# Kernel optimization log

Hardware: AMD Instinct MI355X
Metric: run time of the kernel (lower is better)

The kernel has to match this reference:

```python
import jax, jax.numpy as jnp
import numpy as np

HARDNESS = 5.0

def setup_inputs() -> dict:
    key = jax.random.key(0)
    k1, k2 = jax.random.split(key)
    x = jax.random.normal(k1, (64, 8, 32, 32, 16), dtype=jnp.float32)
    ref = jax.random.normal(k2, (64, 16), dtype=jnp.float32)
    return {"input": x, "ref": ref}

def reference(input, ref):
    # Squared L2 distance from every element vector (last dim) to every codeword,
    x2 = jnp.sum(input * input, axis=-1)                      # (D1,D2,D3,D4)
    r2 = jnp.sum(ref * ref, axis=-1)                          # (M,)
    cross = jnp.einsum('abcde,me->mabcd', input, ref)         # (M,D1,D2,D3,D4)
    sq_l2 = x2[None] - 2.0 * cross + r2[:, None, None, None, None]
    # Softmax over codebook axis with -hardness temperature (dim=0 in torch).
    y = jax.nn.softmax(-HARDNESS * sq_l2, axis=0)             # (M,D1,D2,D3,D4)
    # Weighted combination of codewords.
    z = jnp.einsum('mabcd,me->abcde', y, ref)                 # (D1..D5)
    return z
```

## Files before the change

### kernel.cpp

```cpp
#include <hip/hip_runtime.h>
#include <math.h>

#define CB_M 64
#define CB_D 16
#define HARD 5.0f
#define LOG2E 1.44269504088896340736f

typedef __attribute__((ext_vector_type(8))) short bf16x8;
typedef __attribute__((ext_vector_type(4))) float f32x4;
typedef __attribute__((ext_vector_type(4))) int   i32x4;

#if __has_builtin(__builtin_amdgcn_exp2f)
#define EXP2F(x) __builtin_amdgcn_exp2f(x)
#else
#define EXP2F(x) exp2f(x)
#endif

#if __has_builtin(__builtin_amdgcn_rcpf)
#define RCPF(x) __builtin_amdgcn_rcpf(x)
#else
#define RCPF(x) (1.0f / (x))
#endif

__device__ __forceinline__ ushort f2bf_rne(float f) {
    unsigned u = __float_as_uint(f);
    u += 0x7fffu + ((u >> 16) & 1u);
    return (ushort)(u >> 16);
}
__device__ __forceinline__ float bf2f(ushort h) {
    return __uint_as_float(((unsigned)h) << 16);
}
__device__ __forceinline__ int pk(float a, float b) {
    return (int)__builtin_amdgcn_perm(__float_as_uint(a), __float_as_uint(b), 0x07060302u);
}
__device__ __forceinline__ float rnd(float a) {
    return __uint_as_float(__float_as_uint(a) + 0x8000u);
}
__device__ __forceinline__ float hi_trunc(float a) {
    return __uint_as_float(__float_as_uint(a) & 0xffff0000u);
}

__global__ __launch_bounds__(256, 4) void stq_main(const float* __restrict__ x,
                                                   const float* __restrict__ ref,
                                                   float* __restrict__ out,
                                                   int ntiles) {
    __shared__ __align__(16) float  cb_bias[CB_M];
    __shared__ __align__(16) ushort cb_rs_hi[CB_M][CB_D];
    __shared__ __align__(16) ushort cb_rs_lo[CB_M][CB_D];
    __shared__ __align__(16) ushort cb_rzT_hi[CB_D][CB_M];

    const int tid = threadIdx.x;

    if (tid < CB_M) {
        const f32x4* rp = (const f32x4*)(ref + tid * CB_D);
        f32x4 q0 = rp[0], q1 = rp[1], q2 = rp[2], q3 = rp[3];
        float r[CB_D] = {q0.x,q0.y,q0.z,q0.w, q1.x,q1.y,q1.z,q1.w,
                         q2.x,q2.y,q2.z,q2.w, q3.x,q3.y,q3.z,q3.w};
        float r2 = 0.0f;
#pragma unroll
        for (int j = 0; j < CB_D; ++j) r2 += r[j] * r[j];
        cb_bias[tid] = -(HARD * LOG2E) * r2;
        const float s = 2.0f * HARD * LOG2E;
#pragma unroll
        for (int j = 0; j < CB_D; ++j) {
            float v = s * r[j];
            ushort h = f2bf_rne(v);
            cb_rs_hi[tid][j] = h;
            cb_rs_lo[tid][j] = f2bf_rne(v - bf2f(h));
            cb_rzT_hi[j][tid] = f2bf_rne(r[j]);
        }
    }
    __syncthreads();

    const int lane = tid & 63;
    const int wid  = tid >> 6;
    const int i = lane & 15;
    const int c = lane >> 4;
    const bool hiquad = (c < 2);

    bf16x8 A1[4];
    f32x4  cinit[4];
#pragma unroll
    for (int t = 0; t < 4; ++t) {
        const int cwa = 32 * (t >> 1) + 8 * (i >> 2) + 4 * (t & 1) + (i & 3);
        const ushort* src = hiquad ? &cb_rs_hi[cwa][0] : &cb_rs_lo[cwa][0];
        A1[t] = *(const bf16x8*)(src + (c & 1) * 8);
#pragma unroll
        for (int r = 0; r < 4; ++r)
            cinit[t][r] = cb_bias[32 * (t >> 1) + 8 * c + 4 * (t & 1) + r];
    }
    bf16x8 BzH0 = *(const bf16x8*)&cb_rzT_hi[i][c * 8];
    bf16x8 BzH1 = *(const bf16x8*)&cb_rzT_hi[i][32 + c * 8];

    const int nwaves = gridDim.x * 4;
    int tile = blockIdx.x * 4 + wid;

    f32x4 nxa, nxb;
    {
        const float* xp = x + ((size_t)tile * 16 + i) * CB_D + (c & 1) * 8;
        nxa = *(const f32x4*)xp;
        nxb = *(const f32x4*)(xp + 4);
    }

#pragma unroll 1
    for (; tile < ntiles; tile += nwaves) {
        f32x4 xa = nxa, xb = nxb;
        const int nt = tile + nwaves;
        if (nt < ntiles) {
            const float* xp = x + ((size_t)nt * 16 + i) * CB_D + (c & 1) * 8;
            nxa = *(const f32x4*)xp;
            nxb = *(const f32x4*)(xp + 4);
        }

        i32x4 B1i, B2i;
        B1i.x = pk(xa.y, xa.x); B1i.y = pk(xa.w, xa.z);
        B1i.z = pk(xb.y, xb.x); B1i.w = pk(xb.w, xb.z);
        float l0 = xa.x - hi_trunc(xa.x), l1 = xa.y - hi_trunc(xa.y);
        float l2 = xa.z - hi_trunc(xa.z), l3 = xa.w - hi_trunc(xa.w);
        float l4 = xb.x - hi_trunc(xb.x), l5 = xb.y - hi_trunc(xb.y);
        float l6 = xb.z - hi_trunc(xb.z), l7 = xb.w - hi_trunc(xb.w);
        B2i.x = hiquad ? pk(rnd(l1), rnd(l0)) : 0;
        B2i.y = hiquad ? pk(rnd(l3), rnd(l2)) : 0;
        B2i.z = hiquad ? pk(rnd(l5), rnd(l4)) : 0;
        B2i.w = hiquad ? pk(rnd(l7), rnd(l6)) : 0;
        bf16x8 B1 = __builtin_bit_cast(bf16x8, B1i);
        bf16x8 B2 = __builtin_bit_cast(bf16x8, B2i);

        f32x4 acc[4];
#pragma unroll
        for (int t = 0; t < 4; ++t) {
            acc[t] = __builtin_amdgcn_mfma_f32_16x16x32_bf16(A1[t], B1, cinit[t], 0, 0, 0);
            acc[t] = __builtin_amdgcn_mfma_f32_16x16x32_bf16(A1[t], B2, acc[t], 0, 0, 0);
        }

        float lmax = acc[0][0];
#pragma unroll
        for (int t = 0; t < 4; ++t)
#pragma unroll
            for (int r = 0; r < 4; ++r) lmax = fmaxf(lmax, acc[t][r]);
        lmax = fmaxf(lmax, __shfl_xor(lmax, 16, 64));
        lmax = fmaxf(lmax, __shfl_xor(lmax, 32, 64));

        float lsum = 0.0f;
#pragma unroll
        for (int t = 0; t < 4; ++t)
#pragma unroll
            for (int r = 0; r < 4; ++r) {
                acc[t][r] = EXP2F(acc[t][r] - lmax);
                lsum += acc[t][r];
            }
        lsum += __shfl_xor(lsum, 16, 64);
        lsum += __shfl_xor(lsum, 32, 64);
        const float inv = RCPF(lsum);

        i32x4 P1i, P2i;
        P1i.x = pk(rnd(acc[0][1] * inv), rnd(acc[0][0] * inv));
        P1i.y = pk(rnd(acc[0][3] * inv), rnd(acc[0][2] * inv));
        P1i.z = pk(rnd(acc[1][1] * inv), rnd(acc[1][0] * inv));
        P1i.w = pk(rnd(acc[1][3] * inv), rnd(acc[1][2] * inv));
        P2i.x = pk(rnd(acc[2][1] * inv), rnd(acc[2][0] * inv));
        P2i.y = pk(rnd(acc[2][3] * inv), rnd(acc[2][2] * inv));
        P2i.z = pk(rnd(acc[3][1] * inv), rnd(acc[3][0] * inv));
        P2i.w = pk(rnd(acc[3][3] * inv), rnd(acc[3][2] * inv));
        bf16x8 P1 = __builtin_bit_cast(bf16x8, P1i);
        bf16x8 P2 = __builtin_bit_cast(bf16x8, P2i);

        f32x4 z = {0.0f, 0.0f, 0.0f, 0.0f};
        z = __builtin_amdgcn_mfma_f32_16x16x32_bf16(P1, BzH0, z, 0, 0, 0);
        z = __builtin_amdgcn_mfma_f32_16x16x32_bf16(P2, BzH1, z, 0, 0, 0);

        const int rowbase = tile * 16;
#pragma unroll
        for (int r = 0; r < 4; ++r)
            out[(size_t)(rowbase + 4 * c + r) * CB_D + i] = z[r];
    }
}

extern "C" void kernel_launch(void* const* d_in, const int* in_sizes, int n_in,
                              void* d_out, int out_size, void* d_ws, size_t ws_size,
                              hipStream_t stream) {
    const float* x   = (const float*)d_in[0];
    const float* ref = (const float*)d_in[1];
    float* out = (float*)d_out;

    const int nvec = in_sizes[0] / CB_D;
    const int ntiles = nvec / 16;

    stq_main<<<2048, 256, 0, stream>>>(x, ref, out, ntiles);
}
```

Measured before the change: 87.94 us.

## Process two tiles per wave iteration and defer softmax normalization to output

Each wave now handles a pair of 16-row tiles per loop iteration, interleaving their MFMAs and cross-lane reductions to expose more independent work. The softmax normalization moves from the probabilities to the final output: unnormalized exponentials are packed to bf16 by truncation, and the z results are scaled by a reciprocal fetched via shuffle. Rounding on the residual and probability packing is dropped, and the launch bound is lowered to 3 waves per SIMD to allow more registers. This trades some bf16 precision and occupancy for higher ILP and fewer VALU ops per tile, and an odd tile count would leave the last tile unprocessed.

```diff
diff --git a/kernel.cpp b/kernel.cpp
--- a/kernel.cpp
+++ b/kernel.cpp
@@ -33,14 +33,11 @@
 __device__ __forceinline__ int pk(float a, float b) {
     return (int)__builtin_amdgcn_perm(__float_as_uint(a), __float_as_uint(b), 0x07060302u);
 }
-__device__ __forceinline__ float rnd(float a) {
-    return __uint_as_float(__float_as_uint(a) + 0x8000u);
-}
 __device__ __forceinline__ float hi_trunc(float a) {
     return __uint_as_float(__float_as_uint(a) & 0xffff0000u);
 }
 
-__global__ __launch_bounds__(256, 4) void stq_main(const float* __restrict__ x,
+__global__ __launch_bounds__(256, 3) void stq_main(const float* __restrict__ x,
                                                    const float* __restrict__ ref,
                                                    float* __restrict__ out,
                                                    int ntiles) {
@@ -77,6 +74,7 @@
     const int i = lane & 15;
     const int c = lane >> 4;
     const bool hiquad = (c < 2);
+    const int  bmask = hiquad ? -1 : 0;
 
     bf16x8 A1[4];
     f32x4  cinit[4];
@@ -93,86 +91,128 @@
     bf16x8 BzH1 = *(const bf16x8*)&cb_rzT_hi[i][32 + c * 8];
 
     const int nwaves = gridDim.x * 4;
-    int tile = blockIdx.x * 4 + wid;
-
-    f32x4 nxa, nxb;
+    const int npairs = ntiles >> 1;
+    int p = blockIdx.x * 4 + wid;
+
+    f32x4 nx0a, nx0b, nx1a, nx1b;
     {
-        const float* xp = x + ((size_t)tile * 16 + i) * CB_D + (c & 1) * 8;
-        nxa = *(const f32x4*)xp;
-        nxb = *(const f32x4*)(xp + 4);
+        const float* xp = x + ((size_t)p * 32 + i) * CB_D + (c & 1) * 8;
+        nx0a = *(const f32x4*)xp;
+        nx0b = *(const f32x4*)(xp + 4);
+        nx1a = *(const f32x4*)(xp + 16 * CB_D);
+        nx1b = *(const f32x4*)(xp + 16 * CB_D + 4);
     }
 
 #pragma unroll 1
-    for (; tile < ntiles; tile += nwaves) {
-        f32x4 xa = nxa, xb = nxb;
-        const int nt = tile + nwaves;
-        if (nt < ntiles) {
-            const float* xp = x + ((size_t)nt * 16 + i) * CB_D + (c & 1) * 8;
-            nxa = *(const f32x4*)xp;
-            nxb = *(const f32x4*)(xp + 4);
-        }
-
-        i32x4 B1i, B2i;
-        B1i.x = pk(xa.y, xa.x); B1i.y = pk(xa.w, xa.z);
-        B1i.z = pk(xb.y, xb.x); B1i.w = pk(xb.w, xb.z);
-        float l0 = xa.x - hi_trunc(xa.x), l1 = xa.y - hi_trunc(xa.y);
-        float l2 = xa.z - hi_trunc(xa.z), l3 = xa.w - hi_trunc(xa.w);
-        float l4 = xb.x - hi_trunc(xb.x), l5 = xb.y - hi_trunc(xb.y);
-        float l6 = xb.z - hi_trunc(xb.z), l7 = xb.w - hi_trunc(xb.w);
-        B2i.x = hiquad ? pk(rnd(l1), rnd(l0)) : 0;
-        B2i.y = hiquad ? pk(rnd(l3), rnd(l2)) : 0;
-        B2i.z = hiquad ? pk(rnd(l5), rnd(l4)) : 0;
-        B2i.w = hiquad ? pk(rnd(l7), rnd(l6)) : 0;
-        bf16x8 B1 = __builtin_bit_cast(bf16x8, B1i);
-        bf16x8 B2 = __builtin_bit_cast(bf16x8, B2i);
-
-        f32x4 acc[4];
-#pragma unroll
-        for (int t = 0; t < 4; ++t) {
-            acc[t] = __builtin_amdgcn_mfma_f32_16x16x32_bf16(A1[t], B1, cinit[t], 0, 0, 0);
-            acc[t] = __builtin_amdgcn_mfma_f32_16x16x32_bf16(A1[t], B2, acc[t], 0, 0, 0);
-        }
-
-        float lmax = acc[0][0];
-#pragma unroll
-        for (int t = 0; t < 4; ++t)
-#pragma unroll
-            for (int r = 0; r < 4; ++r) lmax = fmaxf(lmax, acc[t][r]);
-        lmax = fmaxf(lmax, __shfl_xor(lmax, 16, 64));
-        lmax = fmaxf(lmax, __shfl_xor(lmax, 32, 64));
-
-        float lsum = 0.0f;
-#pragma unroll
-        for (int t = 0; t < 4; ++t)
-#pragma unroll
-            for (int r = 0; r < 4; ++r) {
-                acc[t][r] = EXP2F(acc[t][r] - lmax);
-                lsum += acc[t][r];
+    for (; p < npairs; p += nwaves) {
+        f32x4 xa0 = nx0a, xb0 = nx0b, xa1 = nx1a, xb1 = nx1b;
+        const int np_ = p + nwaves;
+        if (np_ < npairs) {
+            const float* xp = x + ((size_t)np_ * 32 + i) * CB_D + (c & 1) * 8;
+            nx0a = *(const f32x4*)xp;
+            nx0b = *(const f32x4*)(xp + 4);
+            nx1a = *(const f32x4*)(xp + 16 * CB_D);
+            nx1b = *(const f32x4*)(xp + 16 * CB_D + 4);
+        }
+
+        bf16x8 B1[2], B2[2];
+        {
+            i32x4 b1, b2;
+            b1.x = pk(xa0.y, xa0.x); b1.y = pk(xa0.w, xa0.z);
+            b1.z = pk(xb0.y, xb0.x); b1.w = pk(xb0.w, xb0.z);
+            b2.x = pk(xa0.y - hi_trunc(xa0.y), xa0.x - hi_trunc(xa0.x)) & bmask;
+            b2.y = pk(xa0.w - hi_trunc(xa0.w), xa0.z - hi_trunc(xa0.z)) & bmask;
+            b2.z = pk(xb0.y - hi_trunc(xb0.y), xb0.x - hi_trunc(xb0.x)) & bmask;
+            b2.w = pk(xb0.w - hi_trunc(xb0.w), xb0.z - hi_trunc(xb0.z)) & bmask;
+            B1[0] = __builtin_bit_cast(bf16x8, b1);
+            B2[0] = __builtin_bit_cast(bf16x8, b2);
+            b1.x = pk(xa1.y, xa1.x); b1.y = pk(xa1.w, xa1.z);
+            b1.z = pk(xb1.y, xb1.x); b1.w = pk(xb1.w, xb1.z);
+            b2.x = pk(xa1.y - hi_trunc(xa1.y), xa1.x - hi_trunc(xa1.x)) & bmask;
+            b2.y = pk(xa1.w - hi_trunc(xa1.w), xa1.z - hi_trunc(xa1.z)) & bmask;
+            b2.z = pk(xb1.y - hi_trunc(xb1.y), xb1.x - hi_trunc(xb1.x)) & bmask;
+            b2.w = pk(xb1.w - hi_trunc(xb1.w), xb1.z - hi_trunc(xb1.z)) & bmask;
+            B1[1] = __builtin_bit_cast(bf16x8, b1);
+            B2[1] = __builtin_bit_cast(bf16x8, b2);
+        }
+
+        f32x4 acc[2][4];
+#pragma unroll
+        for (int u = 0; u < 2; ++u)
+#pragma unroll
+            for (int t = 0; t < 4; ++t) {
+                acc[u][t] = __builtin_amdgcn_mfma_f32_16x16x32_bf16(A1[t], B1[u], cinit[t], 0, 0, 0);
+                acc[u][t] = __builtin_amdgcn_mfma_f32_16x16x32_bf16(A1[t], B2[u], acc[u][t], 0, 0, 0);
             }
-        lsum += __shfl_xor(lsum, 16, 64);
-        lsum += __shfl_xor(lsum, 32, 64);
-        const float inv = RCPF(lsum);
-
-        i32x4 P1i, P2i;
-        P1i.x = pk(rnd(acc[0][1] * inv), rnd(acc[0][0] * inv));
-        P1i.y = pk(rnd(acc[0][3] * inv), rnd(acc[0][2] * inv));
-        P1i.z = pk(rnd(acc[1][1] * inv), rnd(acc[1][0] * inv));
-        P1i.w = pk(rnd(acc[1][3] * inv), rnd(acc[1][2] * inv));
-        P2i.x = pk(rnd(acc[2][1] * inv), rnd(acc[2][0] * inv));
-        P2i.y = pk(rnd(acc[2][3] * inv), rnd(acc[2][2] * inv));
-        P2i.z = pk(rnd(acc[3][1] * inv), rnd(acc[3][0] * inv));
-        P2i.w = pk(rnd(acc[3][3] * inv), rnd(acc[3][2] * inv));
-        bf16x8 P1 = __builtin_bit_cast(bf16x8, P1i);
-        bf16x8 P2 = __builtin_bit_cast(bf16x8, P2i);
-
-        f32x4 z = {0.0f, 0.0f, 0.0f, 0.0f};
-        z = __builtin_amdgcn_mfma_f32_16x16x32_bf16(P1, BzH0, z, 0, 0, 0);
-        z = __builtin_amdgcn_mfma_f32_16x16x32_bf16(P2, BzH1, z, 0, 0, 0);
-
-        const int rowbase = tile * 16;
-#pragma unroll
-        for (int r = 0; r < 4; ++r)
-            out[(size_t)(rowbase + 4 * c + r) * CB_D + i] = z[r];
+
+        float lmax[2];
+#pragma unroll
+        for (int u = 0; u < 2; ++u) {
+            float m01 = fmaxf(fmaxf(acc[u][0][0], acc[u][0][1]), fmaxf(acc[u][0][2], acc[u][0][3]));
+            float m23 = fmaxf(fmaxf(acc[u][1][0], acc[u][1][1]), fmaxf(acc[u][1][2], acc[u][1][3]));
+            float m45 = fmaxf(fmaxf(acc[u][2][0], acc[u][2][1]), fmaxf(acc[u][2][2], acc[u][2][3]));
+            float m67 = fmaxf(fmaxf(acc[u][3][0], acc[u][3][1]), fmaxf(acc[u][3][2], acc[u][3][3]));
+            lmax[u] = fmaxf(fmaxf(m01, m23), fmaxf(m45, m67));
+        }
+        float s0a = __shfl_xor(lmax[0], 16, 64);
+        float s1a = __shfl_xor(lmax[1], 16, 64);
+        lmax[0] = fmaxf(lmax[0], s0a);
+        lmax[1] = fmaxf(lmax[1], s1a);
+        s0a = __shfl_xor(lmax[0], 32, 64);
+        s1a = __shfl_xor(lmax[1], 32, 64);
+        lmax[0] = fmaxf(lmax[0], s0a);
+        lmax[1] = fmaxf(lmax[1], s1a);
+
+        float lsum[2];
+#pragma unroll
+        for (int u = 0; u < 2; ++u) {
+            float s = 0.0f;
+#pragma unroll
+            for (int t = 0; t < 4; ++t)
+#pragma unroll
+                for (int r = 0; r < 4; ++r) {
+                    acc[u][t][r] = EXP2F(acc[u][t][r] - lmax[u]);
+                    s += acc[u][t][r];
+                }
+            lsum[u] = s;
+        }
+        s0a = __shfl_xor(lsum[0], 16, 64);
+        s1a = __shfl_xor(lsum[1], 16, 64);
+        lsum[0] += s0a;
+        lsum[1] += s1a;
+        s0a = __shfl_xor(lsum[0], 32, 64);
+        s1a = __shfl_xor(lsum[1], 32, 64);
+        float inv0 = RCPF(lsum[0] + s0a);
+        float inv1 = RCPF(lsum[1] + s1a);
+
+        f32x4 z[2];
+#pragma unroll
+        for (int u = 0; u < 2; ++u) {
+            i32x4 p1, p2;
+            p1.x = pk(acc[u][0][1], acc[u][0][0]);
+            p1.y = pk(acc[u][0][3], acc[u][0][2]);
+            p1.z = pk(acc[u][1][1], acc[u][1][0]);
+            p1.w = pk(acc[u][1][3], acc[u][1][2]);
+            p2.x = pk(acc[u][2][1], acc[u][2][0]);
+            p2.y = pk(acc[u][2][3], acc[u][2][2]);
+            p2.z = pk(acc[u][3][1], acc[u][3][0]);
+            p2.w = pk(acc[u][3][3], acc[u][3][2]);
+            bf16x8 P1 = __builtin_bit_cast(bf16x8, p1);
+            bf16x8 P2 = __builtin_bit_cast(bf16x8, p2);
+            f32x4 zz = {0.0f, 0.0f, 0.0f, 0.0f};
+            zz = __builtin_amdgcn_mfma_f32_16x16x32_bf16(P1, BzH0, zz, 0, 0, 0);
+            zz = __builtin_amdgcn_mfma_f32_16x16x32_bf16(P2, BzH1, zz, 0, 0, 0);
+            z[u] = zz;
+        }
+
+        const int rowbase = p * 32;
+#pragma unroll
+        for (int r = 0; r < 4; ++r) {
+            float iv0 = __shfl(inv0, 4 * c + r, 64);
+            float iv1 = __shfl(inv1, 4 * c + r, 64);
+            out[(size_t)(rowbase + 4 * c + r) * CB_D + i]      = z[0][r] * iv0;
+            out[(size_t)(rowbase + 16 + 4 * c + r) * CB_D + i] = z[1][r] * iv1;
+        }
     }
 }
 
```

Measured after the change: 87.21 us. Within noise of the previous version (-0.8%).
